# Kernel optimization log

Measured on AMD Instinct MI355X. Metric: run time of the kernel, lower is better.

Reference implementation:

```python
import jax, jax.numpy as jnp
import numpy as np

N = 50000
E = 1600000
HID = 128
K = 2
EPS = 0.3


def setup_inputs() -> dict:
    key = jax.random.key(0)
    ks = jax.random.split(key, 8)
    x = jax.random.normal(ks[0], (N, 512), dtype=jnp.float32)
    edge_index = jax.random.randint(ks[1], (2, E), 0, N, dtype=jnp.int32)
    t1_w = jax.random.normal(ks[2], (HID, 512), dtype=jnp.float32) * (1.414 / np.sqrt(512))
    t1_b = jnp.zeros((HID,), dtype=jnp.float32)
    gate_w = jax.random.normal(ks[3], (K, 2 * HID), dtype=jnp.float32) * (1.414 / np.sqrt(2 * HID))
    gate_b = jnp.zeros((K,), dtype=jnp.float32)
    t2_w = jax.random.normal(ks[4], (40, HID), dtype=jnp.float32) * (1.414 / np.sqrt(HID))
    t2_b = jnp.zeros((40,), dtype=jnp.float32)
    return {"x": x, "edge_index": edge_index, "t1_w": t1_w, "t1_b": t1_b,
            "gate_w": gate_w, "gate_b": gate_b, "t2_w": t2_w, "t2_b": t2_b}


def reference(x, edge_index, t1_w, t1_b, gate_w, gate_b, t2_w, t2_b):
    row, col = edge_index[0], edge_index[1]
    # degree(row, num_nodes=N).clamp(min=1) ** -0.5
    deg = jax.ops.segment_sum(jnp.ones((E,), dtype=x.dtype), row, num_segments=N)
    norm_degree = jnp.clip(deg, 1.0) ** -0.5  # [N]

    h = jax.nn.relu(x @ t1_w.T + t1_b)  # [N, HID]
    raw = h
    for k in range(K):
        # gate(cat([h[row], h[col]], 1)) == h[row] @ W[:H] + h[col] @ W[H:]
        w_r, w_c = gate_w[k, :HID], gate_w[k, HID:]
        g = jnp.tanh(h[row] @ w_r + h[col] @ w_c + gate_b[k])  # [E]
        norm = g * norm_degree[row] * norm_degree[col]          # [E]
        # message: norm * x_j (x_j = h[row], source), scatter-add at col (target)
        agg = jax.ops.segment_sum(norm[:, None] * h[row], col, num_segments=N)
        h = EPS * raw + agg
    logits = h @ t2_w.T + t2_b  # [N, 40]
    return jax.nn.log_softmax(logits, axis=1)
```

## Files before the change

kernel.cpp:

```cpp
#include <hip/hip_runtime.h>
#include <hip/hip_bf16.h>
#include <hip/hip_fp16.h>

#define N_NODES 50000
#define N_EDGES 1600000
#define HIDDEN  128
#define EPS_C   0.3f
#define NWORDS  12500
#define CHUNK   12500
#define NCHUNK  128

typedef _Float16 f16x8 __attribute__((ext_vector_type(8)));
typedef float    f32x16 __attribute__((ext_vector_type(16)));

__global__ __launch_bounds__(256) void k_hist(const int* __restrict__ ei, unsigned int* __restrict__ part) {
    __shared__ unsigned int hist[NWORDS];
    int b = blockIdx.x;
    int type  = b >> 7;
    int chunk = b & 127;
    const int* src = ei + (size_t)type * N_EDGES + (size_t)chunk * CHUNK;
    for (int i = threadIdx.x; i < NWORDS; i += 256) hist[i] = 0;
    __syncthreads();
    for (int i = threadIdx.x; i < CHUNK; i += 256) {
        int v = src[i];
        atomicAdd(&hist[v >> 2], 1u << ((v & 3) * 8));
    }
    __syncthreads();
    unsigned int* dst = part + ((size_t)type * NCHUNK + chunk) * NWORDS;
    for (int i = threadIdx.x; i < NWORDS; i += 256) dst[i] = hist[i];
}

__global__ __launch_bounds__(256) void k_reduce(const unsigned int* __restrict__ part,
                                                float* __restrict__ nd, int* __restrict__ cnt,
                                                unsigned short* __restrict__ cntpre) {
    int w = blockIdx.x * 256 + threadIdx.x;
    if (w >= NWORDS) return;
    unsigned int s0 = 0, s1 = 0, s2 = 0, s3 = 0;
    const unsigned int* dp = part + w;
    for (int b = 0; b < NCHUNK; ++b) {
        unsigned int v = dp[(size_t)b * NWORDS];
        s0 += v & 255u; s1 += (v >> 8) & 255u; s2 += (v >> 16) & 255u; s3 += v >> 24;
    }
    nd[4 * w + 0] = rsqrtf(fmaxf((float)s0, 1.f));
    nd[4 * w + 1] = rsqrtf(fmaxf((float)s1, 1.f));
    nd[4 * w + 2] = rsqrtf(fmaxf((float)s2, 1.f));
    nd[4 * w + 3] = rsqrtf(fmaxf((float)s3, 1.f));
    const unsigned int* cp = part + (size_t)NCHUNK * NWORDS + w;
    unsigned int r0 = 0, r1 = 0, r2 = 0, r3 = 0;
    for (int b = 0; b < NCHUNK; ++b) {
        size_t o = (size_t)b * N_NODES + 4 * w;
        *(ushort4*)&cntpre[o] = make_ushort4((unsigned short)r0, (unsigned short)r1,
                                             (unsigned short)r2, (unsigned short)r3);
        unsigned int v = cp[(size_t)b * NWORDS];
        r0 += v & 255u; r1 += (v >> 8) & 255u; r2 += (v >> 16) & 255u; r3 += v >> 24;
    }
    cnt[4 * w + 0] = (int)r0;
    cnt[4 * w + 1] = (int)r1;
    cnt[4 * w + 2] = (int)r2;
    cnt[4 * w + 3] = (int)r3;
}

__global__ __launch_bounds__(256) void k_scan_a(const int* __restrict__ cnt,
                                                int* __restrict__ out, int* __restrict__ partials) {
    __shared__ int sh[256];
    int t = threadIdx.x;
    int base = blockIdx.x * 1024 + t * 4;
    int v0 = (base + 0 < N_NODES) ? cnt[base + 0] : 0;
    int v1 = (base + 1 < N_NODES) ? cnt[base + 1] : 0;
    int v2 = (base + 2 < N_NODES) ? cnt[base + 2] : 0;
    int v3 = (base + 3 < N_NODES) ? cnt[base + 3] : 0;
    int s = v0 + v1 + v2 + v3;
    sh[t] = s;
    __syncthreads();
    for (int off = 1; off < 256; off <<= 1) {
        int add = (t >= off) ? sh[t - off] : 0;
        __syncthreads();
        sh[t] += add;
        __syncthreads();
    }
    int excl = sh[t] - s;
    if (t == 255) partials[blockIdx.x] = sh[255];
    if (base + 0 < N_NODES) out[base + 0] = excl;
    if (base + 1 < N_NODES) out[base + 1] = excl + v0;
    if (base + 2 < N_NODES) out[base + 2] = excl + v0 + v1;
    if (base + 3 < N_NODES) out[base + 3] = excl + v0 + v1 + v2;
}

__global__ void k_scan_b(int* partials, int* colptr, int nb) {
    if (threadIdx.x == 0 && blockIdx.x == 0) {
        int run = 0;
        for (int i = 0; i < nb; ++i) { int t = partials[i]; partials[i] = run; run += t; }
        colptr[N_NODES] = run;
    }
}

__global__ void k_scan_c(int* __restrict__ colptr, const int* __restrict__ partials) {
    int i = blockIdx.x * blockDim.x + threadIdx.x;
    if (i >= N_NODES) return;
    colptr[i] += partials[i >> 10];
}

__global__ __launch_bounds__(256) void k_scatter2(const int* __restrict__ ei, const int* __restrict__ colptr,
                                                  const unsigned short* __restrict__ cntpre,
                                                  int* __restrict__ csr) {
    __shared__ unsigned int rank[NWORDS];
    int b = blockIdx.x;
    for (int i = threadIdx.x; i < NWORDS; i += 256) rank[i] = 0;
    __syncthreads();
    const int* rs = ei + (size_t)b * CHUNK;
    const int* cs = ei + N_EDGES + (size_t)b * CHUNK;
    const unsigned short* pre = cntpre + (size_t)b * N_NODES;
    for (int i = threadIdx.x; i < CHUNK; i += 256) {
        int r = rs[i];
        int c = cs[i];
        unsigned int old = atomicAdd(&rank[c >> 2], 1u << ((c & 3) * 8));
        unsigned int lr = (old >> ((c & 3) * 8)) & 255u;
        int pos = colptr[c] + (int)pre[c] + (int)lr;
        csr[pos] = r;
    }
}

__global__ void k_cvt(const float4* __restrict__ src, __half2* __restrict__ dst, int n4) {
    int i = blockIdx.x * 256 + threadIdx.x;
    if (i >= n4) return;
    float4 v = src[i];
    dst[2 * i]     = __floats2half2_rn(v.x, v.y);
    dst[2 * i + 1] = __floats2half2_rn(v.z, v.w);
}

__global__ __launch_bounds__(256) void k_gemm1(const float* __restrict__ x, const _Float16* __restrict__ wh,
                                               const float* __restrict__ bias, float* __restrict__ h,
                                               _Float16* __restrict__ hb) {
    int wave = threadIdx.x >> 6;
    int lane = threadIdx.x & 63;
    int mstrip = wave & 1;
    int nstrip = wave >> 1;
    int lm   = lane & 31;
    int half = lane >> 5;

    int m0 = blockIdx.x * 64 + mstrip * 32;
    int m  = m0 + lm;
    int mc = (m < N_NODES) ? m : (N_NODES - 1);
    int n0 = nstrip * 64;

    const float*    arow  = x  + (size_t)mc * 512 + half * 8;
    const _Float16* brow0 = wh + (size_t)(n0 + lm) * 512 + half * 8;
    const _Float16* brow1 = brow0 + (size_t)32 * 512;

    f32x16 acc0, acc1;
#pragma unroll
    for (int i = 0; i < 16; ++i) { acc0[i] = 0.f; acc1[i] = 0.f; }

#pragma unroll 4
    for (int k0 = 0; k0 < 512; k0 += 16) {
        float4 a0 = *(const float4*)(arow + k0);
        float4 a1 = *(const float4*)(arow + k0 + 4);
        f16x8 av;
        av[0] = (_Float16)a0.x; av[1] = (_Float16)a0.y; av[2] = (_Float16)a0.z; av[3] = (_Float16)a0.w;
        av[4] = (_Float16)a1.x; av[5] = (_Float16)a1.y; av[6] = (_Float16)a1.z; av[7] = (_Float16)a1.w;
        f16x8 b0 = *(const f16x8*)(brow0 + k0);
        f16x8 b1 = *(const f16x8*)(brow1 + k0);
        acc0 = __builtin_amdgcn_mfma_f32_32x32x16_f16(av, b0, acc0, 0, 0, 0);
        acc1 = __builtin_amdgcn_mfma_f32_32x32x16_f16(av, b1, acc1, 0, 0, 0);
    }

    float bs0 = bias[n0 + lm];
    float bs1 = bias[n0 + 32 + lm];
#pragma unroll
    for (int reg = 0; reg < 16; ++reg) {
        int row = (reg & 3) + 8 * (reg >> 2) + 4 * half;
        int gm = m0 + row;
        if (gm < N_NODES) {
            float v0 = fmaxf(acc0[reg] + bs0, 0.f);
            float v1 = fmaxf(acc1[reg] + bs1, 0.f);
            h[(size_t)gm * HIDDEN + n0 + lm]      = v0;
            h[(size_t)gm * HIDDEN + n0 + 32 + lm] = v1;
            hb[(size_t)gm * HIDDEN + n0 + lm]      = (_Float16)v0;
            hb[(size_t)gm * HIDDEN + n0 + 32 + lm] = (_Float16)v1;
        }
    }
}

__global__ __launch_bounds__(256) void k_dot(const float* __restrict__ h, const float* __restrict__ gw,
                                             const float* __restrict__ gb, const float* __restrict__ nd,
                                             int layer, float2* __restrict__ dn, float* __restrict__ dcb) {
    int node = blockIdx.x * 4 + (threadIdx.x >> 6);
    int lane = threadIdx.x & 63;
    if (node >= N_NODES) return;
    const float2* hv = (const float2*)h;
    float2 wr = ((const float2*)(gw + layer * 256))[lane];
    float2 wc = ((const float2*)(gw + layer * 256 + 128))[lane];
    float2 hc = hv[(size_t)node * 64 + lane];
    float a = hc.x * wr.x + hc.y * wr.y;
    float b = hc.x * wc.x + hc.y * wc.y;
#pragma unroll
    for (int off = 32; off >= 1; off >>= 1) {
        a += __shfl_xor(a, off, 64);
        b += __shfl_xor(b, off, 64);
    }
    if (lane == 0) {
        dn[node]  = make_float2(a, nd[node]);
        dcb[node] = b + gb[layer];
    }
}

__global__ __launch_bounds__(256) void k_edgew(const int* __restrict__ csr, const int* __restrict__ colptr,
                                               const float2* __restrict__ dn, const float* __restrict__ dcb,
                                               float* __restrict__ warr) {
    int node = blockIdx.x * 4 + (threadIdx.x >> 6);
    int lane = threadIdx.x & 63;
    if (node >= N_NODES) return;
    float dc  = dcb[node];
    int beg = colptr[node], end = colptr[node + 1];
    for (int p = beg + lane; p < end; p += 64) {
        int r = csr[p];
        float2 v = dn[r];
        float xx = v.x + dc;
        float t = __expf(2.0f * xx);
        float g = 1.0f - 2.0f / (t + 1.0f);
        warr[p] = g * v.y;
    }
}

__global__ __launch_bounds__(256) void k_prop(const __half2* __restrict__ hb, const float* __restrict__ raw,
                                              const int* __restrict__ colptr, const int* __restrict__ csr,
                                              const float* __restrict__ warr, const float* __restrict__ nd,
                                              float* __restrict__ hn, __half2* __restrict__ hbn) {
    int lane = threadIdx.x & 63;
    int node = __builtin_amdgcn_readfirstlane(blockIdx.x * 4 + (threadIdx.x >> 6));
    int beg = __builtin_amdgcn_readfirstlane(colptr[node]);
    int end = __builtin_amdgcn_readfirstlane(colptr[node + 1]);
    float acc0 = 0.f, acc1 = 0.f;
    int p = beg;
    for (; p + 8 <= end; p += 8) {
        int r0 = csr[p + 0], r1 = csr[p + 1], r2 = csr[p + 2], r3 = csr[p + 3];
        int r4 = csr[p + 4], r5 = csr[p + 5], r6 = csr[p + 6], r7 = csr[p + 7];
        float w0 = warr[p + 0], w1 = warr[p + 1], w2 = warr[p + 2], w3 = warr[p + 3];
        float w4 = warr[p + 4], w5 = warr[p + 5], w6 = warr[p + 6], w7 = warr[p + 7];
        __half2 v0 = hb[(size_t)r0 * 64 + lane];
        __half2 v1 = hb[(size_t)r1 * 64 + lane];
        __half2 v2 = hb[(size_t)r2 * 64 + lane];
        __half2 v3 = hb[(size_t)r3 * 64 + lane];
        __half2 v4 = hb[(size_t)r4 * 64 + lane];
        __half2 v5 = hb[(size_t)r5 * 64 + lane];
        __half2 v6 = hb[(size_t)r6 * 64 + lane];
        __half2 v7 = hb[(size_t)r7 * 64 + lane];
        acc0 = fmaf(w0, __low2float(v0), acc0);  acc1 = fmaf(w0, __high2float(v0), acc1);
        acc0 = fmaf(w1, __low2float(v1), acc0);  acc1 = fmaf(w1, __high2float(v1), acc1);
        acc0 = fmaf(w2, __low2float(v2), acc0);  acc1 = fmaf(w2, __high2float(v2), acc1);
        acc0 = fmaf(w3, __low2float(v3), acc0);  acc1 = fmaf(w3, __high2float(v3), acc1);
        acc0 = fmaf(w4, __low2float(v4), acc0);  acc1 = fmaf(w4, __high2float(v4), acc1);
        acc0 = fmaf(w5, __low2float(v5), acc0);  acc1 = fmaf(w5, __high2float(v5), acc1);
        acc0 = fmaf(w6, __low2float(v6), acc0);  acc1 = fmaf(w6, __high2float(v6), acc1);
        acc0 = fmaf(w7, __low2float(v7), acc0);  acc1 = fmaf(w7, __high2float(v7), acc1);
    }
    for (; p < end; ++p) {
        int r = csr[p];
        float w = warr[p];
        __half2 v = hb[(size_t)r * 64 + lane];
        acc0 = fmaf(w, __low2float(v), acc0);
        acc1 = fmaf(w, __high2float(v), acc1);
    }
    float ndc = nd[node];
    float2 rw = ((const float2*)raw)[(size_t)node * 64 + lane];
    float2 o;
    o.x = fmaf(EPS_C, rw.x, ndc * acc0);
    o.y = fmaf(EPS_C, rw.y, ndc * acc1);
    if (hn)  ((float2*)hn)[(size_t)node * 64 + lane] = o;
    if (hbn) hbn[(size_t)node * 64 + lane] = __floats2half2_rn(o.x, o.y);
}

__global__ __launch_bounds__(256) void k_out(const float* __restrict__ h, const float* __restrict__ w2,
                                             const float* __restrict__ b2, float* __restrict__ out) {
    __shared__ float w2t[128][40];
    __shared__ float hs[4][128];
    int wid  = threadIdx.x >> 6;
    int lane = threadIdx.x & 63;
    int node = blockIdx.x * 4 + wid;

    for (int idx = threadIdx.x; idx < 40 * 128; idx += 256) {
        int j = idx >> 7;
        int i = idx & 127;
        w2t[i][j] = w2[idx];
    }
    if (node < N_NODES) {
        const float2* hvv = (const float2*)h;
        float2 v = hvv[(size_t)node * 64 + lane];
        hs[wid][2 * lane]     = v.x;
        hs[wid][2 * lane + 1] = v.y;
    }
    __syncthreads();
    if (node < N_NODES) {
        int j = lane;
        float logit = -INFINITY;
        if (j < 40) {
            float a = 0.f;
#pragma unroll 8
            for (int i = 0; i < 128; ++i) a = fmaf(hs[wid][i], w2t[i][j], a);
            logit = a + b2[j];
        }
        float mx = logit;
#pragma unroll
        for (int off = 32; off >= 1; off >>= 1) mx = fmaxf(mx, __shfl_xor(mx, off, 64));
        float ex = (j < 40) ? expf(logit - mx) : 0.f;
        float sum = ex;
#pragma unroll
        for (int off = 32; off >= 1; off >>= 1) sum += __shfl_xor(sum, off, 64);
        float ls = logf(sum);
        if (j < 40) out[(size_t)node * 40 + j] = logit - mx - ls;
    }
}

extern "C" void kernel_launch(void* const* d_in, const int* in_sizes, int n_in,
                              void* d_out, int out_size, void* d_ws, size_t ws_size,
                              hipStream_t stream) {
    const float* x   = (const float*)d_in[0];
    const int*   ei  = (const int*)  d_in[1];
    const float* t1w = (const float*)d_in[2];
    const float* t1b = (const float*)d_in[3];
    const float* gw  = (const float*)d_in[4];
    const float* gb  = (const float*)d_in[5];
    const float* w2  = (const float*)d_in[6];
    const float* b2  = (const float*)d_in[7];
    float* out = (float*)d_out;

    char* p = (char*)d_ws;
    int*    colptr   = (int*)p;    p += (size_t)(N_NODES + 64) * 4;
    int*    partials = (int*)p;    p += 256 * 4;
    float*  nd       = (float*)p;  p += (size_t)N_NODES * 4;
    int*    cnt      = (int*)p;    p += (size_t)N_NODES * 4;
    float*  dcb      = (float*)p;  p += (size_t)N_NODES * 4;
    float2* dn       = (float2*)p; p += (size_t)N_NODES * 8;
    int*    csr      = (int*)p;    p += (size_t)N_EDGES * 4;
    float*  warr     = (float*)p;  p += (size_t)N_EDGES * 4;
    _Float16* wh     = (_Float16*)p; p += (size_t)HIDDEN * 512 * 2;
    char* q = p;
    unsigned int*   part   = (unsigned int*)q;
    unsigned short* cntpre = (unsigned short*)(q + (size_t)2 * NCHUNK * NWORDS * 4);
    __half2* hb0 = (__half2*)p; p += (size_t)N_NODES * 64 * 4;
    __half2* hb1 = (__half2*)p; p += (size_t)N_NODES * 64 * 4;
    float*  h0   = (float*)p;   p += (size_t)N_NODES * HIDDEN * 4;
    float*  h1   = (float*)p;   p += (size_t)N_NODES * HIDDEN * 4;
    float*  h2   = (float*)p;   p += (size_t)N_NODES * HIDDEN * 4;

    k_hist<<<2 * NCHUNK, 256, 0, stream>>>(ei, part);
    k_reduce<<<(NWORDS + 255) / 256, 256, 0, stream>>>(part, nd, cnt, cntpre);
    int nb = (N_NODES + 1023) / 1024;
    k_scan_a<<<nb, 256, 0, stream>>>(cnt, colptr, partials);
    k_scan_b<<<1, 64, 0, stream>>>(partials, colptr, nb);
    k_scan_c<<<(N_NODES + 255) / 256, 256, 0, stream>>>(colptr, partials);
    k_scatter2<<<NCHUNK, 256, 0, stream>>>(ei, colptr, cntpre, csr);

    k_cvt<<<(16384 + 255) / 256, 256, 0, stream>>>((const float4*)t1w, (__half2*)wh, 16384);
    k_gemm1<<<(N_NODES + 63) / 64, 256, 0, stream>>>(x, wh, t1b, h0, (_Float16*)hb0);

    k_dot  <<<(N_NODES + 3) / 4, 256, 0, stream>>>(h0, gw, gb, nd, 0, dn, dcb);
    k_edgew<<<(N_NODES + 3) / 4, 256, 0, stream>>>(csr, colptr, dn, dcb, warr);
    k_prop <<<(N_NODES + 3) / 4, 256, 0, stream>>>(hb0, h0, colptr, csr, warr, nd, h1, hb1);

    k_dot  <<<(N_NODES + 3) / 4, 256, 0, stream>>>(h1, gw, gb, nd, 1, dn, dcb);
    k_edgew<<<(N_NODES + 3) / 4, 256, 0, stream>>>(csr, colptr, dn, dcb, warr);
    k_prop <<<(N_NODES + 3) / 4, 256, 0, stream>>>(hb1, h0, colptr, csr, warr, nd, h2, (__half2*)nullptr);

    k_out<<<(N_NODES + 3) / 4, 256, 0, stream>>>(h2, w2, b2, out);
}
```

Baseline: 559.2 us.

## Stage GEMM tiles through swizzled LDS with prefetch; use half-wave per node in edgew

The first linear layer now loads 64x64 tiles of x and the weights cooperatively into XOR-swizzled shared memory, converting x to fp16 once per tile, and prefetches the next K tile into registers while MFMAs run. Previously each wave streamed its own rows straight from global memory, so x rows were loaded twice per block and weights many times. Separately, the edge-weight kernel assigns 32 lanes per node instead of 64, which suits the average in-degree of about 32 and leaves fewer lanes idle. The cost is extra LDS traffic and two barriers per K step.

```diff
diff --git a/kernel.cpp b/kernel.cpp
--- a/kernel.cpp
+++ b/kernel.cpp
@@ -11,6 +11,7 @@
 #define NCHUNK  128
 
 typedef _Float16 f16x8 __attribute__((ext_vector_type(8)));
+typedef _Float16 f16x4 __attribute__((ext_vector_type(4)));
 typedef float    f32x16 __attribute__((ext_vector_type(16)));
 
 __global__ __launch_bounds__(256) void k_hist(const int* __restrict__ ei, unsigned int* __restrict__ part) {
@@ -131,45 +132,84 @@
 __global__ __launch_bounds__(256) void k_gemm1(const float* __restrict__ x, const _Float16* __restrict__ wh,
                                                const float* __restrict__ bias, float* __restrict__ h,
                                                _Float16* __restrict__ hb) {
-    int wave = threadIdx.x >> 6;
-    int lane = threadIdx.x & 63;
+    __shared__ _Float16 As[64 * 64];
+    __shared__ _Float16 Bs[128 * 64];
+    int t = threadIdx.x;
+    int wave = t >> 6;
+    int lane = t & 63;
+    int lm   = lane & 31;
+    int half = lane >> 5;
     int mstrip = wave & 1;
     int nstrip = wave >> 1;
-    int lm   = lane & 31;
-    int half = lane >> 5;
-
-    int m0 = blockIdx.x * 64 + mstrip * 32;
-    int m  = m0 + lm;
-    int mc = (m < N_NODES) ? m : (N_NODES - 1);
-    int n0 = nstrip * 64;
-
-    const float*    arow  = x  + (size_t)mc * 512 + half * 8;
-    const _Float16* brow0 = wh + (size_t)(n0 + lm) * 512 + half * 8;
-    const _Float16* brow1 = brow0 + (size_t)32 * 512;
+
+    int m0  = blockIdx.x * 64;
+    int wm0 = m0 + mstrip * 32;
+    int n0  = nstrip * 64;
+
+    int aidx[4], arow[4], ac4[4];
+    int bidx, brow[4], bg[4];
+#pragma unroll
+    for (int i = 0; i < 4; ++i) {
+        aidx[i] = i * 256 + t;
+        arow[i] = aidx[i] >> 4;
+        ac4[i]  = aidx[i] & 15;
+        bidx    = i * 256 + t;
+        brow[i] = bidx >> 3;
+        bg[i]   = bidx & 7;
+    }
+
+    float4 pa[4];
+    f16x8  pb[4];
+#define LOAD_TILES(K0)                                                                    \
+    {                                                                                     \
+        _Pragma("unroll")                                                                 \
+        for (int i = 0; i < 4; ++i) {                                                     \
+            int gr = m0 + arow[i]; if (gr >= N_NODES) gr = N_NODES - 1;                   \
+            pa[i] = *(const float4*)(x + (size_t)gr * 512 + (K0) + ac4[i] * 4);           \
+            pb[i] = *(const f16x8*)(wh + (size_t)brow[i] * 512 + (K0) + bg[i] * 8);       \
+        }                                                                                 \
+    }
 
     f32x16 acc0, acc1;
 #pragma unroll
     for (int i = 0; i < 16; ++i) { acc0[i] = 0.f; acc1[i] = 0.f; }
 
-#pragma unroll 4
-    for (int k0 = 0; k0 < 512; k0 += 16) {
-        float4 a0 = *(const float4*)(arow + k0);
-        float4 a1 = *(const float4*)(arow + k0 + 4);
-        f16x8 av;
-        av[0] = (_Float16)a0.x; av[1] = (_Float16)a0.y; av[2] = (_Float16)a0.z; av[3] = (_Float16)a0.w;
-        av[4] = (_Float16)a1.x; av[5] = (_Float16)a1.y; av[6] = (_Float16)a1.z; av[7] = (_Float16)a1.w;
-        f16x8 b0 = *(const f16x8*)(brow0 + k0);
-        f16x8 b1 = *(const f16x8*)(brow1 + k0);
-        acc0 = __builtin_amdgcn_mfma_f32_32x32x16_f16(av, b0, acc0, 0, 0, 0);
-        acc1 = __builtin_amdgcn_mfma_f32_32x32x16_f16(av, b1, acc1, 0, 0, 0);
-    }
+    int ar = mstrip * 32 + lm;
+    int brA = n0 + lm;
+    int brB = n0 + 32 + lm;
+
+    LOAD_TILES(0);
+    for (int k0 = 0; k0 < 512; k0 += 64) {
+#pragma unroll
+        for (int i = 0; i < 4; ++i) {
+            f16x4 a;
+            a[0] = (_Float16)pa[i].x; a[1] = (_Float16)pa[i].y;
+            a[2] = (_Float16)pa[i].z; a[3] = (_Float16)pa[i].w;
+            int g = ac4[i] >> 1;
+            *(f16x4*)&As[arow[i] * 64 + (((g ^ (arow[i] & 7)) << 3)) + (ac4[i] & 1) * 4] = a;
+            *(f16x8*)&Bs[brow[i] * 64 + ((bg[i] ^ (brow[i] & 7)) << 3)] = pb[i];
+        }
+        __syncthreads();
+        if (k0 + 64 < 512) LOAD_TILES(k0 + 64);
+#pragma unroll
+        for (int kk = 0; kk < 4; ++kk) {
+            int ag = kk * 2 + half;
+            f16x8 av  = *(const f16x8*)&As[ar  * 64 + ((ag ^ (ar  & 7)) << 3)];
+            f16x8 bv0 = *(const f16x8*)&Bs[brA * 64 + ((ag ^ (brA & 7)) << 3)];
+            f16x8 bv1 = *(const f16x8*)&Bs[brB * 64 + ((ag ^ (brA & 7)) << 3)];
+            acc0 = __builtin_amdgcn_mfma_f32_32x32x16_f16(av, bv0, acc0, 0, 0, 0);
+            acc1 = __builtin_amdgcn_mfma_f32_32x32x16_f16(av, bv1, acc1, 0, 0, 0);
+        }
+        __syncthreads();
+    }
+#undef LOAD_TILES
 
     float bs0 = bias[n0 + lm];
     float bs1 = bias[n0 + 32 + lm];
 #pragma unroll
     for (int reg = 0; reg < 16; ++reg) {
         int row = (reg & 3) + 8 * (reg >> 2) + 4 * half;
-        int gm = m0 + row;
+        int gm = wm0 + row;
         if (gm < N_NODES) {
             float v0 = fmaxf(acc0[reg] + bs0, 0.f);
             float v1 = fmaxf(acc1[reg] + bs1, 0.f);
@@ -207,12 +247,12 @@
 __global__ __launch_bounds__(256) void k_edgew(const int* __restrict__ csr, const int* __restrict__ colptr,
                                                const float2* __restrict__ dn, const float* __restrict__ dcb,
                                                float* __restrict__ warr) {
-    int node = blockIdx.x * 4 + (threadIdx.x >> 6);
-    int lane = threadIdx.x & 63;
+    int node = blockIdx.x * 8 + (threadIdx.x >> 5);
+    int sl   = threadIdx.x & 31;
     if (node >= N_NODES) return;
     float dc  = dcb[node];
     int beg = colptr[node], end = colptr[node + 1];
-    for (int p = beg + lane; p < end; p += 64) {
+    for (int p = beg + sl; p < end; p += 32) {
         int r = csr[p];
         float2 v = dn[r];
         float xx = v.x + dc;
@@ -355,11 +395,11 @@
     k_gemm1<<<(N_NODES + 63) / 64, 256, 0, stream>>>(x, wh, t1b, h0, (_Float16*)hb0);
 
     k_dot  <<<(N_NODES + 3) / 4, 256, 0, stream>>>(h0, gw, gb, nd, 0, dn, dcb);
-    k_edgew<<<(N_NODES + 3) / 4, 256, 0, stream>>>(csr, colptr, dn, dcb, warr);
+    k_edgew<<<(N_NODES + 7) / 8, 256, 0, stream>>>(csr, colptr, dn, dcb, warr);
     k_prop <<<(N_NODES + 3) / 4, 256, 0, stream>>>(hb0, h0, colptr, csr, warr, nd, h1, hb1);
 
     k_dot  <<<(N_NODES + 3) / 4, 256, 0, stream>>>(h1, gw, gb, nd, 1, dn, dcb);
-    k_edgew<<<(N_NODES + 3) / 4, 256, 0, stream>>>(csr, colptr, dn, dcb, warr);
+    k_edgew<<<(N_NODES + 7) / 8, 256, 0, stream>>>(csr, colptr, dn, dcb, warr);
     k_prop <<<(N_NODES + 3) / 4, 256, 0, stream>>>(hb1, h0, colptr, csr, warr, nd, h2, (__half2*)nullptr);
 
     k_out<<<(N_NODES + 3) / 4, 256, 0, stream>>>(h2, w2, b2, out);
```

Result: faster. 518.6 us (-7.3%).
